# Optimization experiments

Measured on AMD Instinct MI355X. Metric: run time of the kernel, lower is better.

## Reference

```python
import jax, jax.numpy as jnp
import numpy as np

NUM_VARS = 10
HID = 256
INP = 4
B = 32
T = 64

_adj = np.ones((NUM_VARS, NUM_VARS)) - np.eye(NUM_VARS)
SEND, RECV = np.where(_adj)          # each [E], E = num_vars*(num_vars-1) = 90
E = len(SEND)
_e2n = np.zeros((NUM_VARS, E), dtype=np.float32)
_e2n[RECV, np.arange(E)] = 1.0       # encode_onehot(recv).T -> [num_vars, E]
E2N = jnp.asarray(_e2n)
SEND_J = jnp.asarray(SEND)
RECV_J = jnp.asarray(RECV)


def _mlp_block(x, w1, b1, w2, b2, gamma, beta):
    # RefNRIMLP: elu(fc1) -> (dropout p=0) -> elu(fc2) -> batchnorm over view(-1, H)
    h = jax.nn.elu(x @ w1 + b1)
    h = jax.nn.elu(h @ w2 + b2)
    mu = h.mean(axis=(0, 1, 2), keepdims=True)
    var = h.var(axis=(0, 1, 2), keepdims=True)
    return gamma * (h - mu) * jax.lax.rsqrt(var + 1e-5) + beta


def setup_inputs() -> dict:
    key = jax.random.key(0)
    ks = jax.random.split(key, 12)

    def xavier(k, fi, fo):
        return jax.random.normal(k, (fi, fo), jnp.float32) * np.sqrt(2.0 / (fi + fo))

    d = {
        "x": jax.random.normal(ks[0], (B, T, NUM_VARS, INP), jnp.float32),
        # mlp1: inp -> hid -> hid
        "w1a": xavier(ks[1], INP, HID), "b1a": jnp.full((HID,), 0.1),
        "w1b": xavier(ks[2], HID, HID), "b1b": jnp.full((HID,), 0.1),
        "g1": jnp.ones((HID,)), "be1": jnp.zeros((HID,)),
        # mlp2: 2*hid -> hid -> hid
        "w2a": xavier(ks[3], 2 * HID, HID), "b2a": jnp.full((HID,), 0.1),
        "w2b": xavier(ks[4], HID, HID), "b2b": jnp.full((HID,), 0.1),
        "g2": jnp.ones((HID,)), "be2": jnp.zeros((HID,)),
        # mlp3: hid -> hid -> hid
        "w3a": xavier(ks[5], HID, HID), "b3a": jnp.full((HID,), 0.1),
        "w3b": xavier(ks[6], HID, HID), "b3b": jnp.full((HID,), 0.1),
        "g3": jnp.ones((HID,)), "be3": jnp.zeros((HID,)),
        # output heads
        "wo1": xavier(ks[7], HID, HID), "bo1": jnp.full((HID,), 0.1),
        "wo2": xavier(ks[8], HID, 1), "bo2": jnp.full((1,), 0.1),
    }
    return d


def reference(x, w1a, b1a, w1b, b1b, g1, be1,
              w2a, b2a, w2b, b2b, g2, be2,
              w3a, b3a, w3b, b3b, g3, be3,
              wo1, bo1, wo2, bo2):
    # x: [B, T, N, INP] -> transpose(2,1): [B, N, T, INP]
    h = jnp.transpose(x, (0, 2, 1, 3))
    h = _mlp_block(h, w1a, b1a, w1b, b1b, g1, be1)            # [B, N, T, H]
    # node2edge: gather senders/receivers along node dim, concat on features
    e = jnp.concatenate([h[:, SEND_J], h[:, RECV_J]], axis=-1)  # [B, E, T, 2H]
    e = _mlp_block(e, w2a, b2a, w2b, b2b, g2, be2)            # [B, E, T, H]
    # edge2node: incidence matmul over edge dim, normalize by in-degree
    n = jnp.einsum('ve,betH->bvtH', E2N, e) / (NUM_VARS - 1)   # [B, N, T, H]
    n = _mlp_block(n, w3a, b3a, w3b, b3b, g3, be3)
    n = jax.nn.relu(n) @ wo1 + bo1
    n = jax.nn.relu(n) @ wo2 + bo2                             # [B, N, T, 1]
    out = jnp.transpose(n, (0, 2, 1, 3)).mean(axis=-1)         # [B, T, N]
    return out
```

## Files before the change

### kernel.cpp

```cpp
#include <hip/hip_runtime.h>
#include <hip/hip_bf16.h>
#include <cstdint>

#define DI __device__ __forceinline__

typedef short bf16x8 __attribute__((ext_vector_type(8)));
typedef float f32x4 __attribute__((ext_vector_type(4)));
typedef unsigned short u16;
typedef unsigned short u16x8 __attribute__((ext_vector_type(8)));

static constexpr int NV = 10, NE = 90, TT = 64;
static constexpr int R1 = 20480;
static constexpr int R2 = 184320;

DI float bf2f(u16 u) { union { unsigned int i; float f; } x; x.i = ((unsigned int)u) << 16; return x.f; }
DI u16 f2bf(float f) { unsigned int u = __float_as_uint(f); return (u16)((u + 0x7FFF + ((u >> 16) & 1)) >> 16); }
DI float elu(float v) { return v > 0.f ? v : __expf(v) - 1.f; }

#define GLL(srcp, dstp) __builtin_amdgcn_global_load_lds( \
    (const __attribute__((address_space(1))) unsigned int*)(srcp), \
    (__attribute__((address_space(3))) unsigned int*)(dstp), 16, 0, 0)

__global__ __launch_bounds__(256) void pack4(
    const float* __restrict__ s0, u16* __restrict__ d0,
    const float* __restrict__ s1, u16* __restrict__ d1,
    const float* __restrict__ s2, u16* __restrict__ d2,
    const float* __restrict__ s3, u16* __restrict__ d3) {
    const float* s; u16* d;
    switch (blockIdx.y) {
        case 0: s = s0; d = d0; break;
        case 1: s = s1; d = d1; break;
        case 2: s = s2; d = d2; break;
        default: s = s3; d = d3; break;
    }
    int tid = threadIdx.x;
    int bn = blockIdx.x >> 3, kt = blockIdx.x & 7;
#pragma unroll
    for (int p = 0; p < 2; ++p) {
        int n = bn * 128 + p * 64 + (tid >> 2);
        int k = kt * 32 + (tid & 3) * 8;
        u16x8 pk;
#pragma unroll
        for (int e = 0; e < 8; ++e) pk[e] = f2bf(s[(size_t)(k + e) * 256 + n]);
        *(u16x8*)(d + ((size_t)((bn * 8 + kt) * 2 + p)) * 2048 + (size_t)tid * 8) = pk;
    }
}

__global__ __launch_bounds__(256) void pack256(const float* __restrict__ s,
                                               u16* __restrict__ d) {
    int kt = blockIdx.x;
#pragma unroll
    for (int h = 0; h < 2; ++h) {
        int tid2 = threadIdx.x + h * 256;
#pragma unroll
        for (int p = 0; p < 2; ++p) {
            int n = p * 128 + (tid2 >> 2);
            int k = kt * 32 + (tid2 & 3) * 8;
            u16x8 pk;
#pragma unroll
            for (int e = 0; e < 8; ++e) pk[e] = f2bf(s[(size_t)(k + e) * 256 + n]);
            *(u16x8*)(d + ((size_t)(kt * 2 + p)) * 4096 + (size_t)tid2 * 8) = pk;
        }
    }
}

__global__ __launch_bounds__(256) void pack256_w2a(const float* __restrict__ w2a,
                                                   const float* __restrict__ scsh1,
                                                   u16* __restrict__ d) {
    int kt = blockIdx.x;
#pragma unroll
    for (int h = 0; h < 2; ++h) {
        int tid2 = threadIdx.x + h * 256;
#pragma unroll
        for (int p = 0; p < 2; ++p) {
            int n = p * 128 + (tid2 >> 2);
            int k = kt * 32 + (tid2 & 3) * 8;
            u16x8 pk;
#pragma unroll
            for (int e = 0; e < 8; ++e)
                pk[e] = f2bf(scsh1[(k + e) & 255] * w2a[(size_t)(k + e) * 256 + n]);
            *(u16x8*)(d + ((size_t)(kt * 2 + p)) * 4096 + (size_t)tid2 * 8) = pk;
        }
    }
}

__global__ void zero_stats(float* p, int n) {
    int i = blockIdx.x * 256 + threadIdx.x;
    if (i < n) p[i] = 0.f;
}

__global__ void conv_wo2(const float* __restrict__ src, u16* __restrict__ dst) {
    dst[threadIdx.x] = f2bf(src[threadIdx.x]);
}

__global__ __launch_bounds__(256) void fold_b2a(const float* __restrict__ w2a,
                                                const float* __restrict__ scsh1,
                                                const float* __restrict__ b2a,
                                                float* __restrict__ b2aF) {
    __shared__ float red[256];
    int n = blockIdx.x, tid = threadIdx.x;
    float sc = scsh1[256 + tid];
    float s = sc * w2a[tid * 256 + n] + sc * w2a[(tid + 256) * 256 + n];
    red[tid] = s;
    __syncthreads();
    for (int off2 = 128; off2 > 0; off2 >>= 1) {
        if (tid < off2) red[tid] += red[tid + off2];
        __syncthreads();
    }
    if (tid == 0) b2aF[n] = red[0] + b2a[n];
}

__global__ void stats_final(const float* __restrict__ sums, const float* __restrict__ g,
                            const float* __restrict__ be, float invR, float* __restrict__ scsh) {
    int c = threadIdx.x;
    float mu = sums[c] * invR;
    float var = sums[256 + c] * invR - mu * mu;
    float rs = rsqrtf(var + 1e-5f);
    float sc = g[c] * rs;
    scsh[c] = sc;
    scsh[256 + c] = be[c] - mu * sc;
}

__global__ __launch_bounds__(256) void mlp1_fc1(const float* __restrict__ x,
                                                const float* __restrict__ w1a,
                                                const float* __restrict__ b1a,
                                                u16* __restrict__ ha) {
    int tid = threadIdx.x;
    int row = blockIdx.x * 8 + (tid >> 5);
    int ch8 = (tid & 31) * 8;
    int b = row / (NV * TT);
    int v = (row >> 6) % NV;
    int t = row & 63;
    const float* xp = x + ((size_t)(b * TT + t) * NV + v) * 4;
    float x0 = xp[0], x1 = xp[1], x2 = xp[2], x3 = xp[3];
    u16x8 pack;
#pragma unroll
    for (int e = 0; e < 8; ++e) {
        int c = ch8 + e;
        float acc = b1a[c] + x0 * w1a[c] + x1 * w1a[256 + c] + x2 * w1a[512 + c] + x3 * w1a[768 + c];
        pack[e] = f2bf(elu(acc));
    }
    *(u16x8*)(ha + (size_t)row * 256 + ch8) = pack;
}

template <int ACT, bool STATS>
__global__ __launch_bounds__(256) void gemm_kernel(const u16* __restrict__ A,
                                                   const u16* __restrict__ Wt,
                                                   const float* __restrict__ bias,
                                                   u16* __restrict__ out,
                                                   int K,
                                                   float* __restrict__ stats) {
    __shared__ u16 As[3][128 * 32];
    __shared__ u16 Bs[3][128 * 32];
    const int tid = threadIdx.x;
    const int lane = tid & 63, wid = tid >> 6;

    int bm, bn;
    {
        int bid = blockIdx.x;
        int xcd = bid & 7, slot = bid >> 3;
        bn = slot & 1;
        bm = xcd + 8 * (slot >> 1);
    }
    const int m0 = bm * 128, n0 = bn * 128;
    const int wm = wid >> 1, wn = wid & 1;

    const int srow = tid >> 2;
    const int scol8 = (tid & 3) * 8;

    size_t abase0 = (size_t)(m0 + srow) * K;
    size_t abase1 = (size_t)(m0 + srow + 64) * K;
    const int NT = K >> 5;
    const size_t bnbase = (size_t)bn * NT * 4096;

    f32x4 acc[4][4];
#pragma unroll
    for (int i = 0; i < 4; ++i)
#pragma unroll
        for (int j = 0; j < 4; ++j) acc[i][j] = (f32x4)0.f;

    const int lrow = lane & 15;
    const int lk8 = (lane >> 4) * 8;

    auto stage = [&](int bf, int k0) {
        const size_t btile = bnbase + (size_t)(k0 >> 5) * 4096 + (size_t)tid * 8;
        GLL(A + abase0 + k0 + scol8, &As[bf][(wid * 64) * 8]);
        GLL(Wt + btile, &Bs[bf][(wid * 64) * 8]);
        GLL(A + abase1 + k0 + scol8, &As[bf][(256 + wid * 64) * 8]);
        GLL(Wt + btile + 2048, &Bs[bf][(256 + wid * 64) * 8]);
    };

    stage(0, 0);
    stage(1, 32);
    for (int kt = 0; kt < NT; ++kt) {
        if (kt + 1 < NT) {
            asm volatile("s_waitcnt vmcnt(4)" ::: "memory");
        } else {
            asm volatile("s_waitcnt vmcnt(0)" ::: "memory");
        }
        __builtin_amdgcn_s_barrier();
        if (kt + 2 < NT) stage((kt + 2) % 3, (kt + 2) * 32);
        __builtin_amdgcn_sched_barrier(0);
        const int buf = kt % 3;
        bf16x8 a[4], b[4];
#pragma unroll
        for (int i = 0; i < 4; ++i)
            a[i] = *(const bf16x8*)&As[buf][(wm * 64 + i * 16 + lrow) * 32 + lk8];
#pragma unroll
        for (int j = 0; j < 4; ++j)
            b[j] = *(const bf16x8*)&Bs[buf][(wn * 64 + j * 16 + lrow) * 32 + lk8];
#pragma unroll
        for (int i = 0; i < 4; ++i)
#pragma unroll
            for (int j = 0; j < 4; ++j)
                acc[i][j] = __builtin_amdgcn_mfma_f32_16x16x32_bf16(a[i], b[j], acc[i][j], 0, 0, 0);
    }

    float bv[4], sv[4], qv[4];
#pragma unroll
    for (int j = 0; j < 4; ++j) {
        bv[j] = bias[n0 + wn * 64 + j * 16 + lrow];
        if constexpr (STATS) { sv[j] = 0.f; qv[j] = 0.f; }
    }
#pragma unroll
    for (int i = 0; i < 4; ++i) {
#pragma unroll
        for (int j = 0; j < 4; ++j) {
            int col = n0 + wn * 64 + j * 16 + lrow;
#pragma unroll
            for (int r = 0; r < 4; ++r) {
                int row = m0 + wm * 64 + i * 16 + (lane >> 4) * 4 + r;
                float v = acc[i][j][r] + bv[j];
                v = (ACT == 1) ? elu(v) : (v > 0.f ? v : 0.f);
                if constexpr (STATS) { sv[j] += v; qv[j] += v * v; }
                out[(size_t)row * 256 + col] = f2bf(v);
            }
        }
    }
    if constexpr (STATS) {
#pragma unroll
        for (int j = 0; j < 4; ++j) {
            float s = sv[j], q_ = qv[j];
            s += __shfl_xor(s, 16); q_ += __shfl_xor(q_, 16);
            s += __shfl_xor(s, 32); q_ += __shfl_xor(q_, 32);
            if ((lane >> 4) == 0) {
                int col = n0 + wn * 64 + j * 16 + lrow;
                atomicAdd(&stats[col], s);
                atomicAdd(&stats[256 + col], q_);
            }
        }
    }
}

__global__ __launch_bounds__(512) void mlp2_fused(const u16* __restrict__ A,
                                                  const u16* __restrict__ PB1,
                                                  const float* __restrict__ bias1,
                                                  const u16* __restrict__ PB2,
                                                  const float* __restrict__ bias2,
                                                  u16* __restrict__ out,
                                                  float* __restrict__ stats) {
    __shared__ u16 As[3][128 * 32];
    __shared__ u16 Bs[3][256 * 32];
    __shared__ u16 H1[128 * 256];

    const int tid = threadIdx.x;
    const int lane = tid & 63, wid = tid >> 6;

    int bid = blockIdx.x;
    int xcd = bid & 7, slot = bid >> 3;
    int batch = xcd + 8 * (slot / 45);
    int bm = batch * 45 + (slot % 45);
    const int m0 = bm * 128;
    const int wm = wid >> 2, wn = wid & 3;

    size_t sb, rb;
    {
        int m = m0 + (tid >> 2);
        int t = m & 63, be = m >> 6, e = be % NE, b = be / NE;
        int s = e / 9, kk = e - s * 9, r = kk + (kk >= s ? 1 : 0);
        sb = ((size_t)((b * NV + s) * TT + t)) * 256 + (tid & 3) * 8;
        rb = ((size_t)((b * NV + r) * TT + t)) * 256 + (tid & 3) * 8;
    }

    const int lrow = lane & 15;
    const int lk8 = (lane >> 4) * 8;

    f32x4 acc[4][4];
#pragma unroll
    for (int i = 0; i < 4; ++i)
#pragma unroll
        for (int j = 0; j < 4; ++j) acc[i][j] = (f32x4)0.f;

    auto stage1 = [&](int bf, int k0) {
        GLL(A + (k0 < 256 ? sb : rb) + (k0 & 255), &As[bf][tid * 8]);
        const u16* b_ = PB1 + (size_t)(k0 >> 5) * 8192 + (size_t)tid * 8;
        GLL(b_, &Bs[bf][tid * 8]);
        GLL(b_ + 4096, &Bs[bf][4096 + tid * 8]);
    };

    stage1(0, 0);
    stage1(1, 32);
    for (int kt = 0; kt < 16; ++kt) {
        if (kt + 1 < 16) {
            asm volatile("s_waitcnt vmcnt(3)" ::: "memory");
        } else {
            asm volatile("s_waitcnt vmcnt(0)" ::: "memory");
        }
        __builtin_amdgcn_s_barrier();
        if (kt + 2 < 16) stage1((kt + 2) % 3, (kt + 2) * 32);
        __builtin_amdgcn_sched_barrier(0);
        const int buf = kt % 3;
        bf16x8 a[4], b[4];
#pragma unroll
        for (int i = 0; i < 4; ++i)
            a[i] = *(const bf16x8*)&As[buf][(wm * 64 + i * 16 + lrow) * 32 + lk8];
#pragma unroll
        for (int j = 0; j < 4; ++j)
            b[j] = *(const bf16x8*)&Bs[buf][(wn * 64 + j * 16 + lrow) * 32 + lk8];
#pragma unroll
        for (int i = 0; i < 4; ++i)
#pragma unroll
            for (int j = 0; j < 4; ++j)
                acc[i][j] = __builtin_amdgcn_mfma_f32_16x16x32_bf16(a[i], b[j], acc[i][j], 0, 0, 0);
    }

#pragma unroll
    for (int j = 0; j < 4; ++j) {
        int c = wn * 64 + j * 16 + lrow;
        float bv = bias1[c];
        int gx = c >> 3;
        int cl = c & 7;
#pragma unroll
        for (int i = 0; i < 4; ++i) {
#pragma unroll
            for (int r = 0; r < 4; ++r) {
                int m = wm * 64 + i * 16 + (lane >> 4) * 4 + r;
                float v = elu(acc[i][j][r] + bv);
                H1[m * 256 + ((gx ^ (m & 7)) << 3) + cl] = f2bf(v);
            }
        }
    }
    __syncthreads();

#pragma unroll
    for (int i = 0; i < 4; ++i)
#pragma unroll
        for (int j = 0; j < 4; ++j) acc[i][j] = (f32x4)0.f;

    auto stage2 = [&](int bf, int k0) {
        const u16* b_ = PB2 + (size_t)(k0 >> 5) * 8192 + (size_t)tid * 8;
        GLL(b_, &Bs[bf][tid * 8]);
        GLL(b_ + 4096, &Bs[bf][4096 + tid * 8]);
    };

    stage2(0, 0);
    stage2(1, 32);
    for (int kt = 0; kt < 8; ++kt) {
        if (kt + 1 < 8) {
            asm volatile("s_waitcnt vmcnt(2)" ::: "memory");
        } else {
            asm volatile("s_waitcnt vmcnt(0)" ::: "memory");
        }
        __builtin_amdgcn_s_barrier();
        if (kt + 2 < 8) stage2((kt + 2) % 3, (kt + 2) * 32);
        __builtin_amdgcn_sched_barrier(0);
        const int buf = kt % 3;
        const int k0 = kt * 32;
        bf16x8 a[4], b[4];
#pragma unroll
        for (int i = 0; i < 4; ++i) {
            int mr = wm * 64 + i * 16 + lrow;
            int gx = (k0 >> 3) + (lane >> 4);
            a[i] = *(const bf16x8*)&H1[mr * 256 + ((gx ^ (mr & 7)) << 3)];
        }
#pragma unroll
        for (int j = 0; j < 4; ++j)
            b[j] = *(const bf16x8*)&Bs[buf][(wn * 64 + j * 16 + lrow) * 32 + lk8];
#pragma unroll
        for (int i = 0; i < 4; ++i)
#pragma unroll
            for (int j = 0; j < 4; ++j)
                acc[i][j] = __builtin_amdgcn_mfma_f32_16x16x32_bf16(a[i], b[j], acc[i][j], 0, 0, 0);
    }

    float bv2[4], sv[4], qv[4];
#pragma unroll
    for (int j = 0; j < 4; ++j) {
        bv2[j] = bias2[wn * 64 + j * 16 + lrow];
        sv[j] = 0.f;
        qv[j] = 0.f;
    }
#pragma unroll
    for (int i = 0; i < 4; ++i) {
#pragma unroll
        for (int j = 0; j < 4; ++j) {
            int col = wn * 64 + j * 16 + lrow;
#pragma unroll
            for (int r = 0; r < 4; ++r) {
                int row = m0 + wm * 64 + i * 16 + (lane >> 4) * 4 + r;
                float v = elu(acc[i][j][r] + bv2[j]);
                sv[j] += v;
                qv[j] += v * v;
                out[(size_t)row * 256 + col] = f2bf(v);
            }
        }
    }
#pragma unroll
    for (int j = 0; j < 4; ++j) {
        float s = sv[j], q_ = qv[j];
        s += __shfl_xor(s, 16); q_ += __shfl_xor(q_, 16);
        s += __shfl_xor(s, 32); q_ += __shfl_xor(q_, 32);
        if ((lane >> 4) == 0) {
            int col = wn * 64 + j * 16 + lrow;
            atomicAdd(&stats[col], s);
            atomicAdd(&stats[256 + col], q_);
        }
    }
}

__global__ __launch_bounds__(256) void norm_affine_relu(const u16* __restrict__ in,
                                                        const float* __restrict__ scsh,
                                                        u16* __restrict__ out, int n8) {
    int i = blockIdx.x * 256 + threadIdx.x;
    if (i >= n8) return;
    size_t base = (size_t)i * 8;
    int ch8 = (int)(base & 255);
    u16x8 v = *(const u16x8*)(in + base);
    u16x8 o;
#pragma unroll
    for (int e = 0; e < 8; ++e) {
        float f = bf2f(v[e]);
        f = scsh[ch8 + e] * f + scsh[256 + ch8 + e];
        o[e] = f2bf(f > 0.f ? f : 0.f);
    }
    *(u16x8*)(out + base) = o;
}

__global__ __launch_bounds__(256) void edge2node(const u16* __restrict__ h2,
                                                 const float* __restrict__ scsh2,
                                                 u16* __restrict__ n1) {
    int tid = threadIdx.x;
    int row = blockIdx.x * 8 + (tid >> 5);
    int ch8 = (tid & 31) * 8;
    int t = row & 63;
    int bv = row >> 6;
    int v = bv % NV;
    int b = bv / NV;
    float acc[8] = {0, 0, 0, 0, 0, 0, 0, 0};
#pragma unroll
    for (int i = 0; i < 9; ++i) {
        int s = i + (i >= v ? 1 : 0);
        int e = s * 9 + (v < s ? v : v - 1);
        u16x8 vv = *(const u16x8*)(h2 + ((size_t)((b * NE + e) * TT + t)) * 256 + ch8);
#pragma unroll
        for (int k = 0; k < 8; ++k) acc[k] += bf2f(vv[k]);
    }
    const float inv9 = 1.f / 9.f;
    u16x8 o;
#pragma unroll
    for (int k = 0; k < 8; ++k) {
        int c = ch8 + k;
        o[k] = f2bf(scsh2[c] * (acc[k] * inv9) + scsh2[256 + c]);
    }
    *(u16x8*)(n1 + (size_t)row * 256 + ch8) = o;
}

__global__ __launch_bounds__(256) void head2(const u16* __restrict__ a2,
                                             const u16* __restrict__ wo2t,
                                             const float* __restrict__ bo2,
                                             float* __restrict__ out) {
    int tid = threadIdx.x;
    int row = blockIdx.x * 8 + (tid >> 5);
    int l32 = tid & 31;
    int ch8 = l32 * 8;
    u16x8 a = *(const u16x8*)(a2 + (size_t)row * 256 + ch8);
    u16x8 w = *(const u16x8*)(wo2t + ch8);
    float p = 0.f;
#pragma unroll
    for (int k = 0; k < 8; ++k) p += bf2f(a[k]) * bf2f(w[k]);
#pragma unroll
    for (int off = 16; off > 0; off >>= 1) p += __shfl_down(p, off, 32);
    if (l32 == 0) {
        int b = row / (NV * TT);
        int v = (row >> 6) % NV;
        int t = row & 63;
        out[(size_t)(b * TT + t) * NV + v] = p + bo2[0];
    }
}

extern "C" void kernel_launch(void* const* d_in, const int* in_sizes, int n_in,
                              void* d_out, int out_size, void* d_ws, size_t ws_size,
                              hipStream_t stream) {
    const float* x   = (const float*)d_in[0];
    const float* w1a = (const float*)d_in[1];
    const float* b1a = (const float*)d_in[2];
    const float* w1b = (const float*)d_in[3];
    const float* b1b = (const float*)d_in[4];
    const float* g1  = (const float*)d_in[5];
    const float* be1 = (const float*)d_in[6];
    const float* w2a = (const float*)d_in[7];
    const float* b2a = (const float*)d_in[8];
    const float* w2b = (const float*)d_in[9];
    const float* b2b = (const float*)d_in[10];
    const float* g2  = (const float*)d_in[11];
    const float* be2 = (const float*)d_in[12];
    const float* w3a = (const float*)d_in[13];
    const float* b3a = (const float*)d_in[14];
    const float* w3b = (const float*)d_in[15];
    const float* b3b = (const float*)d_in[16];
    const float* g3  = (const float*)d_in[17];
    const float* be3 = (const float*)d_in[18];
    const float* wo1 = (const float*)d_in[19];
    const float* bo1 = (const float*)d_in[20];
    const float* wo2 = (const float*)d_in[21];
    const float* bo2 = (const float*)d_in[22];
    float* out = (float*)d_out;

    char* ws = (char*)d_ws;
    size_t off = 0;
    auto alloc = [&](size_t bytes) {
        void* p = ws + off;
        off = (off + bytes + 255) & ~(size_t)255;
        return p;
    };
    u16* w1bP = (u16*)alloc(2 * 8 * 4096 * 2);
    u16* w3aP = (u16*)alloc(2 * 8 * 4096 * 2);
    u16* w3bP = (u16*)alloc(2 * 8 * 4096 * 2);
    u16* wo1P = (u16*)alloc(2 * 8 * 4096 * 2);
    u16* w2aP = (u16*)alloc(16 * 8192 * 2);
    u16* w2bP = (u16*)alloc(8 * 8192 * 2);
    u16* wo2T = (u16*)alloc(256 * 2);
    float* sums  = (float*)alloc(3 * 512 * 4);
    float* scsh1 = (float*)alloc(512 * 4);
    float* scsh2 = (float*)alloc(512 * 4);
    float* scsh3 = (float*)alloc(512 * 4);
    float* b2aF  = (float*)alloc(256 * 4);
    u16* S0 = (u16*)alloc((size_t)R1 * 256 * 2);
    u16* S1 = (u16*)alloc((size_t)R1 * 256 * 2);
    u16* S2 = (u16*)alloc((size_t)R1 * 256 * 2);
    u16* BIG2 = (u16*)alloc((size_t)R2 * 256 * 2);

    dim3 pgrid(16, 4);
    pack4<<<pgrid, 256, 0, stream>>>(w1b, w1bP, w3a, w3aP, w3b, w3bP, wo1, wo1P);
    pack256<<<8, 256, 0, stream>>>(w2b, w2bP);
    zero_stats<<<6, 256, 0, stream>>>(sums, 3 * 512);
    conv_wo2<<<1, 256, 0, stream>>>(wo2, wo2T);

    mlp1_fc1<<<R1 / 8, 256, 0, stream>>>(x, w1a, b1a, S0);
    gemm_kernel<1, true><<<(R1 / 128) * 2, 256, 0, stream>>>(S0, w1bP, b1b, S1, 256, sums);
    stats_final<<<1, 256, 0, stream>>>(sums, g1, be1, 1.f / R1, scsh1);
    pack256_w2a<<<16, 256, 0, stream>>>(w2a, scsh1, w2aP);
    fold_b2a<<<256, 256, 0, stream>>>(w2a, scsh1, b2a, b2aF);

    mlp2_fused<<<R2 / 128, 512, 0, stream>>>(S1, w2aP, b2aF, w2bP, b2b, BIG2, sums + 512);
    stats_final<<<1, 256, 0, stream>>>(sums + 512, g2, be2, 1.f / R2, scsh2);

    edge2node<<<R1 / 8, 256, 0, stream>>>(BIG2, scsh2, S0);

    gemm_kernel<1, false><<<(R1 / 128) * 2, 256, 0, stream>>>(S0, w3aP, b3a, S1, 256, nullptr);
    gemm_kernel<1, true><<<(R1 / 128) * 2, 256, 0, stream>>>(S1, w3bP, b3b, S2, 256, sums + 1024);
    stats_final<<<1, 256, 0, stream>>>(sums + 1024, g3, be3, 1.f / R1, scsh3);

    norm_affine_relu<<<(R1 * 32 + 255) / 256, 256, 0, stream>>>(S2, scsh3, S0, R1 * 32);
    gemm_kernel<2, false><<<(R1 / 128) * 2, 256, 0, stream>>>(S0, wo1P, bo1, S1, 256, nullptr);
    head2<<<R1 / 8, 256, 0, stream>>>(S1, wo2T, bo2, out);
}
```

Measured before the change: 244.9 us.

## Shrink mlp2_fused tile to 64 rows with 256 threads and double buffering

The fused edge MLP kernel now uses 64-row tiles and 4 waves per block instead of 128 rows and 8 waves, which doubles the block count and reduces LDS use. The triple-buffered pipeline with explicit vmcnt waits is replaced by plain double buffering with __syncthreads. The first fc2 weight tile is prefetched during the fc1 epilogue. This targets occupancy and better block distribution, but each block reloads the full weight matrices for half as many rows, so weight traffic per row doubles, and the simpler synchronisation may expose more load latency.

```diff
diff --git a/kernel.cpp b/kernel.cpp
--- a/kernel.cpp
+++ b/kernel.cpp
@@ -252,26 +252,26 @@
     }
 }
 
-__global__ __launch_bounds__(512) void mlp2_fused(const u16* __restrict__ A,
+__global__ __launch_bounds__(256) void mlp2_fused(const u16* __restrict__ A,
                                                   const u16* __restrict__ PB1,
                                                   const float* __restrict__ bias1,
                                                   const u16* __restrict__ PB2,
                                                   const float* __restrict__ bias2,
                                                   u16* __restrict__ out,
                                                   float* __restrict__ stats) {
-    __shared__ u16 As[3][128 * 32];
-    __shared__ u16 Bs[3][256 * 32];
-    __shared__ u16 H1[128 * 256];
+    __shared__ u16 As[2][64 * 32];
+    __shared__ u16 Bs[2][256 * 32];
+    __shared__ u16 H1[64 * 256];
 
     const int tid = threadIdx.x;
     const int lane = tid & 63, wid = tid >> 6;
 
     int bid = blockIdx.x;
     int xcd = bid & 7, slot = bid >> 3;
-    int batch = xcd + 8 * (slot / 45);
-    int bm = batch * 45 + (slot % 45);
-    const int m0 = bm * 128;
-    const int wm = wid >> 2, wn = wid & 3;
+    int batch = xcd + 8 * (slot / 90);
+    int bm = batch * 90 + (slot % 90);
+    const int m0 = bm * 64;
+    const int wn = wid;
 
     size_t sb, rb;
     {
@@ -293,27 +293,27 @@
 
     auto stage1 = [&](int bf, int k0) {
         GLL(A + (k0 < 256 ? sb : rb) + (k0 & 255), &As[bf][tid * 8]);
-        const u16* b_ = PB1 + (size_t)(k0 >> 5) * 8192 + (size_t)tid * 8;
-        GLL(b_, &Bs[bf][tid * 8]);
-        GLL(b_ + 4096, &Bs[bf][4096 + tid * 8]);
+        const u16* b_ = PB1 + (size_t)(k0 >> 5) * 8192;
+#pragma unroll
+        for (int q = 0; q < 4; ++q)
+            GLL(b_ + (q * 256 + tid) * 8, &Bs[bf][(q * 256 + tid) * 8]);
     };
+    auto stage2 = [&](int bf, int k0) {
+        const u16* b_ = PB2 + (size_t)(k0 >> 5) * 8192;
+#pragma unroll
+        for (int q = 0; q < 4; ++q)
+            GLL(b_ + (q * 256 + tid) * 8, &Bs[bf][(q * 256 + tid) * 8]);
+    };
 
     stage1(0, 0);
-    stage1(1, 32);
+    __syncthreads();
     for (int kt = 0; kt < 16; ++kt) {
-        if (kt + 1 < 16) {
-            asm volatile("s_waitcnt vmcnt(3)" ::: "memory");
-        } else {
-            asm volatile("s_waitcnt vmcnt(0)" ::: "memory");
-        }
-        __builtin_amdgcn_s_barrier();
-        if (kt + 2 < 16) stage1((kt + 2) % 3, (kt + 2) * 32);
-        __builtin_amdgcn_sched_barrier(0);
-        const int buf = kt % 3;
+        if (kt + 1 < 16) stage1((kt + 1) & 1, (kt + 1) * 32);
+        const int buf = kt & 1;
         bf16x8 a[4], b[4];
 #pragma unroll
         for (int i = 0; i < 4; ++i)
-            a[i] = *(const bf16x8*)&As[buf][(wm * 64 + i * 16 + lrow) * 32 + lk8];
+            a[i] = *(const bf16x8*)&As[buf][(i * 16 + lrow) * 32 + lk8];
 #pragma unroll
         for (int j = 0; j < 4; ++j)
             b[j] = *(const bf16x8*)&Bs[buf][(wn * 64 + j * 16 + lrow) * 32 + lk8];
@@ -322,7 +322,11 @@
 #pragma unroll
             for (int j = 0; j < 4; ++j)
                 acc[i][j] = __builtin_amdgcn_mfma_f32_16x16x32_bf16(a[i], b[j], acc[i][j], 0, 0, 0);
-    }
+        __syncthreads();
+    }
+
+    stage2(0, 0);
+    __builtin_amdgcn_sched_barrier(0);
 
 #pragma unroll
     for (int j = 0; j < 4; ++j) {
@@ -334,7 +338,7 @@
         for (int i = 0; i < 4; ++i) {
 #pragma unroll
             for (int r = 0; r < 4; ++r) {
-                int m = wm * 64 + i * 16 + (lane >> 4) * 4 + r;
+                int m = i * 16 + (lane >> 4) * 4 + r;
                 float v = elu(acc[i][j][r] + bv);
                 H1[m * 256 + ((gx ^ (m & 7)) << 3) + cl] = f2bf(v);
             }
@@ -347,29 +351,14 @@
 #pragma unroll
         for (int j = 0; j < 4; ++j) acc[i][j] = (f32x4)0.f;
 
-    auto stage2 = [&](int bf, int k0) {
-        const u16* b_ = PB2 + (size_t)(k0 >> 5) * 8192 + (size_t)tid * 8;
-        GLL(b_, &Bs[bf][tid * 8]);
-        GLL(b_ + 4096, &Bs[bf][4096 + tid * 8]);
-    };
-
-    stage2(0, 0);
-    stage2(1, 32);
     for (int kt = 0; kt < 8; ++kt) {
-        if (kt + 1 < 8) {
-            asm volatile("s_waitcnt vmcnt(2)" ::: "memory");
-        } else {
-            asm volatile("s_waitcnt vmcnt(0)" ::: "memory");
-        }
-        __builtin_amdgcn_s_barrier();
-        if (kt + 2 < 8) stage2((kt + 2) % 3, (kt + 2) * 32);
-        __builtin_amdgcn_sched_barrier(0);
-        const int buf = kt % 3;
+        if (kt + 1 < 8) stage2((kt + 1) & 1, (kt + 1) * 32);
+        const int buf = kt & 1;
         const int k0 = kt * 32;
         bf16x8 a[4], b[4];
 #pragma unroll
         for (int i = 0; i < 4; ++i) {
-            int mr = wm * 64 + i * 16 + lrow;
+            int mr = i * 16 + lrow;
             int gx = (k0 >> 3) + (lane >> 4);
             a[i] = *(const bf16x8*)&H1[mr * 256 + ((gx ^ (mr & 7)) << 3)];
         }
@@ -381,6 +370,7 @@
 #pragma unroll
             for (int j = 0; j < 4; ++j)
                 acc[i][j] = __builtin_amdgcn_mfma_f32_16x16x32_bf16(a[i], b[j], acc[i][j], 0, 0, 0);
+        __syncthreads();
     }
 
     float bv2[4], sv[4], qv[4];
@@ -397,7 +387,7 @@
             int col = wn * 64 + j * 16 + lrow;
 #pragma unroll
             for (int r = 0; r < 4; ++r) {
-                int row = m0 + wm * 64 + i * 16 + (lane >> 4) * 4 + r;
+                int row = m0 + i * 16 + (lane >> 4) * 4 + r;
                 float v = elu(acc[i][j][r] + bv2[j]);
                 sv[j] += v;
                 qv[j] += v * v;
@@ -552,7 +542,7 @@
     pack256_w2a<<<16, 256, 0, stream>>>(w2a, scsh1, w2aP);
     fold_b2a<<<256, 256, 0, stream>>>(w2a, scsh1, b2a, b2aF);
 
-    mlp2_fused<<<R2 / 128, 512, 0, stream>>>(S1, w2aP, b2aF, w2bP, b2b, BIG2, sums + 512);
+    mlp2_fused<<<R2 / 64, 256, 0, stream>>>(S1, w2aP, b2aF, w2bP, b2b, BIG2, sums + 512);
     stats_final<<<1, 256, 0, stream>>>(sums + 512, g2, be2, 1.f / R2, scsh2);
 
     edge2node<<<R1 / 8, 256, 0, stream>>>(BIG2, scsh2, S0);
```

Measured after the change: 252.3 us. 3.0% more time.

## Swizzle LDS tiles in fused edge MLP and prefetch fc2 weights early

Applied to the files above, without the earlier changes.

Repacks the w2a/w2b weight tiles and the gathered A rows with an XOR chunk swizzle so that MFMA fragment reads from shared memory avoid bank conflicts, and updates the read indexing to match. It also issues the first two fc2 weight-tile loads right after the fc1 loop, before the ELU/H1 epilogue, so those loads overlap the epilogue work. This adds an extra barrier, and the packing kernels and the consumer kernel must agree exactly on the swizzle.

```diff
diff --git a/kernel.cpp b/kernel.cpp
--- a/kernel.cpp
+++ b/kernel.cpp
@@ -46,41 +46,37 @@
     }
 }
 
-__global__ __launch_bounds__(256) void pack256(const float* __restrict__ s,
-                                               u16* __restrict__ d) {
+__global__ __launch_bounds__(256) void pack256s(const float* __restrict__ s,
+                                                u16* __restrict__ d) {
     int kt = blockIdx.x;
 #pragma unroll
-    for (int h = 0; h < 2; ++h) {
+    for (int h = 0; h < 4; ++h) {
         int tid2 = threadIdx.x + h * 256;
-#pragma unroll
-        for (int p = 0; p < 2; ++p) {
-            int n = p * 128 + (tid2 >> 2);
-            int k = kt * 32 + (tid2 & 3) * 8;
-            u16x8 pk;
-#pragma unroll
-            for (int e = 0; e < 8; ++e) pk[e] = f2bf(s[(size_t)(k + e) * 256 + n]);
-            *(u16x8*)(d + ((size_t)(kt * 2 + p)) * 4096 + (size_t)tid2 * 8) = pk;
-        }
-    }
-}
-
-__global__ __launch_bounds__(256) void pack256_w2a(const float* __restrict__ w2a,
-                                                   const float* __restrict__ scsh1,
-                                                   u16* __restrict__ d) {
+        int n = tid2 >> 2;
+        int g = (tid2 & 3) ^ ((tid2 >> 2) & 3);
+        int k = kt * 32 + g * 8;
+        u16x8 pk;
+#pragma unroll
+        for (int e = 0; e < 8; ++e) pk[e] = f2bf(s[(size_t)(k + e) * 256 + n]);
+        *(u16x8*)(d + (size_t)kt * 8192 + (size_t)tid2 * 8) = pk;
+    }
+}
+
+__global__ __launch_bounds__(256) void pack256s_w2a(const float* __restrict__ w2a,
+                                                    const float* __restrict__ scsh1,
+                                                    u16* __restrict__ d) {
     int kt = blockIdx.x;
 #pragma unroll
-    for (int h = 0; h < 2; ++h) {
+    for (int h = 0; h < 4; ++h) {
         int tid2 = threadIdx.x + h * 256;
-#pragma unroll
-        for (int p = 0; p < 2; ++p) {
-            int n = p * 128 + (tid2 >> 2);
-            int k = kt * 32 + (tid2 & 3) * 8;
-            u16x8 pk;
-#pragma unroll
-            for (int e = 0; e < 8; ++e)
-                pk[e] = f2bf(scsh1[(k + e) & 255] * w2a[(size_t)(k + e) * 256 + n]);
-            *(u16x8*)(d + ((size_t)(kt * 2 + p)) * 4096 + (size_t)tid2 * 8) = pk;
-        }
+        int n = tid2 >> 2;
+        int g = (tid2 & 3) ^ ((tid2 >> 2) & 3);
+        int k = kt * 32 + g * 8;
+        u16x8 pk;
+#pragma unroll
+        for (int e = 0; e < 8; ++e)
+            pk[e] = f2bf(scsh1[(k + e) & 255] * w2a[(size_t)(k + e) * 256 + n]);
+        *(u16x8*)(d + (size_t)kt * 8192 + (size_t)tid2 * 8) = pk;
     }
 }
 
@@ -278,12 +274,13 @@
         int m = m0 + (tid >> 2);
         int t = m & 63, be = m >> 6, e = be % NE, b = be / NE;
         int s = e / 9, kk = e - s * 9, r = kk + (kk >= s ? 1 : 0);
-        sb = ((size_t)((b * NV + s) * TT + t)) * 256 + (tid & 3) * 8;
-        rb = ((size_t)((b * NV + r) * TT + t)) * 256 + (tid & 3) * 8;
+        int achk = (tid & 3) ^ ((tid >> 2) & 3);
+        sb = ((size_t)((b * NV + s) * TT + t)) * 256 + achk * 8;
+        rb = ((size_t)((b * NV + r) * TT + t)) * 256 + achk * 8;
     }
 
     const int lrow = lane & 15;
-    const int lk8 = (lane >> 4) * 8;
+    const int lsw = (((lane >> 4) ^ (lrow & 3))) * 8;
 
     f32x4 acc[4][4];
 #pragma unroll
@@ -294,6 +291,11 @@
     auto stage1 = [&](int bf, int k0) {
         GLL(A + (k0 < 256 ? sb : rb) + (k0 & 255), &As[bf][tid * 8]);
         const u16* b_ = PB1 + (size_t)(k0 >> 5) * 8192 + (size_t)tid * 8;
+        GLL(b_, &Bs[bf][tid * 8]);
+        GLL(b_ + 4096, &Bs[bf][4096 + tid * 8]);
+    };
+    auto stage2 = [&](int bf, int k0) {
+        const u16* b_ = PB2 + (size_t)(k0 >> 5) * 8192 + (size_t)tid * 8;
         GLL(b_, &Bs[bf][tid * 8]);
         GLL(b_ + 4096, &Bs[bf][4096 + tid * 8]);
     };
@@ -313,16 +315,21 @@
         bf16x8 a[4], b[4];
 #pragma unroll
         for (int i = 0; i < 4; ++i)
-            a[i] = *(const bf16x8*)&As[buf][(wm * 64 + i * 16 + lrow) * 32 + lk8];
+            a[i] = *(const bf16x8*)&As[buf][(wm * 64 + i * 16 + lrow) * 32 + lsw];
 #pragma unroll
         for (int j = 0; j < 4; ++j)
-            b[j] = *(const bf16x8*)&Bs[buf][(wn * 64 + j * 16 + lrow) * 32 + lk8];
+            b[j] = *(const bf16x8*)&Bs[buf][(wn * 64 + j * 16 + lrow) * 32 + lsw];
 #pragma unroll
         for (int i = 0; i < 4; ++i)
 #pragma unroll
             for (int j = 0; j < 4; ++j)
                 acc[i][j] = __builtin_amdgcn_mfma_f32_16x16x32_bf16(a[i], b[j], acc[i][j], 0, 0, 0);
     }
+
+    __builtin_amdgcn_s_barrier();
+    stage2(0, 0);
+    stage2(1, 32);
+    __builtin_amdgcn_sched_barrier(0);
 
 #pragma unroll
     for (int j = 0; j < 4; ++j) {
@@ -347,14 +354,6 @@
 #pragma unroll
         for (int j = 0; j < 4; ++j) acc[i][j] = (f32x4)0.f;
 
-    auto stage2 = [&](int bf, int k0) {
-        const u16* b_ = PB2 + (size_t)(k0 >> 5) * 8192 + (size_t)tid * 8;
-        GLL(b_, &Bs[bf][tid * 8]);
-        GLL(b_ + 4096, &Bs[bf][4096 + tid * 8]);
-    };
-
-    stage2(0, 0);
-    stage2(1, 32);
     for (int kt = 0; kt < 8; ++kt) {
         if (kt + 1 < 8) {
             asm volatile("s_waitcnt vmcnt(2)" ::: "memory");
@@ -375,7 +374,7 @@
         }
 #pragma unroll
         for (int j = 0; j < 4; ++j)
-            b[j] = *(const bf16x8*)&Bs[buf][(wn * 64 + j * 16 + lrow) * 32 + lk8];
+            b[j] = *(const bf16x8*)&Bs[buf][(wn * 64 + j * 16 + lrow) * 32 + lsw];
 #pragma unroll
         for (int i = 0; i < 4; ++i)
 #pragma unroll
@@ -542,14 +541,14 @@
 
     dim3 pgrid(16, 4);
     pack4<<<pgrid, 256, 0, stream>>>(w1b, w1bP, w3a, w3aP, w3b, w3bP, wo1, wo1P);
-    pack256<<<8, 256, 0, stream>>>(w2b, w2bP);
+    pack256s<<<8, 256, 0, stream>>>(w2b, w2bP);
     zero_stats<<<6, 256, 0, stream>>>(sums, 3 * 512);
     conv_wo2<<<1, 256, 0, stream>>>(wo2, wo2T);
 
     mlp1_fc1<<<R1 / 8, 256, 0, stream>>>(x, w1a, b1a, S0);
     gemm_kernel<1, true><<<(R1 / 128) * 2, 256, 0, stream>>>(S0, w1bP, b1b, S1, 256, sums);
     stats_final<<<1, 256, 0, stream>>>(sums, g1, be1, 1.f / R1, scsh1);
-    pack256_w2a<<<16, 256, 0, stream>>>(w2a, scsh1, w2aP);
+    pack256s_w2a<<<16, 256, 0, stream>>>(w2a, scsh1, w2aP);
     fold_b2a<<<256, 256, 0, stream>>>(w2a, scsh1, b2a, b2aF);
 
     mlp2_fused<<<R2 / 128, 512, 0, stream>>>(S1, w2aP, b2aF, w2bP, b2b, BIG2, sums + 512);
```

After: 249.4 us. No clear change (+1.8%).
